# Kernel optimization log

Hardware: AMD Instinct MI355X
Metric: run time of the kernel (lower is better)

Reference implementation:

```python
import jax, jax.numpy as jnp
import numpy as np

B, H, S, D = 1, 16, 2048, 64

def setup_inputs() -> dict:
    key = jax.random.key(0)
    kq, kk, kv = jax.random.split(key, 3)
    q = jax.random.normal(kq, (B, H, S, D), dtype=jnp.float32)
    k = jax.random.normal(kk, (B, H, S, D), dtype=jnp.float32)
    v = jax.random.normal(kv, (B, H, S, D), dtype=jnp.float32)
    return {"q": q, "k": k, "v": v}

def reference(q, k, v):
    # Non-flash Attend forward: causal=True, no mask/bias/prev_attn, dropout=0 (eval)
    dtype = q.dtype
    scale = q.shape[-1] ** -0.5
    # dots: [b, h, i, j]
    dots = jnp.einsum('bhid,bhjd->bhij', q, k) * scale
    i = dots.shape[-2]
    j = dots.shape[-1]
    # create_casual_mask: triu(j - i + 1) -> True where j_idx > i_idx + (j - i)
    causal_mask = jnp.triu(jnp.ones((i, j), dtype=bool), k=j - i + 1)
    mask_value = -jnp.finfo(dtype).max
    dots = jnp.where(causal_mask, mask_value, dots)
    # attn_fn = softmax in float32 (qk_norm=False), cast back to input dtype
    attn = jax.nn.softmax(dots.astype(jnp.float32), axis=-1).astype(dtype)
    out = jnp.einsum('bhij,bhjd->bhid', attn, v)
    return out
```

## Files before the change

### kernel.cpp

```cpp
#include <hip/hip_runtime.h>
#include <hip/hip_bf16.h>
#include <math.h>

#define SEQ 2048
#define NH  16
#define HD  64
#define NW  4

typedef __attribute__((ext_vector_type(8)))  short bf16x8;
typedef __attribute__((ext_vector_type(4)))  float f32x4;
typedef __attribute__((ext_vector_type(16))) float f32x16;

static __device__ inline short f2bf(float f) {
  union { float f; unsigned u; } x; x.f = f;
  unsigned u = x.u;
  unsigned r = (u + 0x7fffu + ((u >> 16) & 1u)) >> 16;
  return (short)r;
}
static __device__ inline unsigned pack2(float e, float o) {
  union { __hip_bfloat162 h; unsigned u; } c;
  c.h = __float22bfloat162_rn(make_float2(e, o));
  return c.u;
}
static __device__ inline bf16x8 cvt8(float4 a, float4 b) {
  union { __hip_bfloat162 h[4]; bf16x8 v; } u;
  u.h[0] = __float22bfloat162_rn(make_float2(a.x, a.y));
  u.h[1] = __float22bfloat162_rn(make_float2(a.z, a.w));
  u.h[2] = __float22bfloat162_rn(make_float2(b.x, b.y));
  u.h[3] = __float22bfloat162_rn(make_float2(b.z, b.w));
  return u.v;
}

__global__ __launch_bounds__(256) void conv_kv_kernel(
    const float* __restrict__ K, const float* __restrict__ V,
    short* __restrict__ Kf, short* __restrict__ Vf) {
  __shared__ short tile[64][72];
  const int h = blockIdx.y;
  const int t64 = blockIdx.x;
  const int tid = threadIdx.x;
  const int c = tid >> 6;
  const int lane = tid & 63;
  const int ql = lane & 31;
  const int hi = lane >> 5;

#pragma unroll
  for (int half = 0; half < 2; ++half) {
    const int t32 = t64 * 2 + half;
    const float* src = K + ((size_t)(h * SEQ + t32 * 32 + ql)) * HD + c * 16 + hi * 8;
    float4 a = *(const float4*)src;
    float4 b = *(const float4*)(src + 4);
    *(bf16x8*)(Kf + (((size_t)(h * 64 + t32) * 4 + c) * 64 + lane) * 8) = cvt8(a, b);
  }
  {
    const int r = tid >> 2, c0 = (tid & 3) * 16;
    const float* vs = V + ((size_t)(h * SEQ + t64 * 64 + r)) * HD + c0;
    float4 a0 = *(const float4*)(vs);
    float4 b0 = *(const float4*)(vs + 4);
    float4 a1 = *(const float4*)(vs + 8);
    float4 b1 = *(const float4*)(vs + 12);
    *(bf16x8*)&tile[r][c0]     = cvt8(a0, b0);
    *(bf16x8*)&tile[r][c0 + 8] = cvt8(a1, b1);
  }
  __syncthreads();
#pragma unroll
  for (int dt = 0; dt < 2; ++dt) {
    const int d = dt * 32 + ql;
    bf16x8 o;
#pragma unroll
    for (int j = 0; j < 8; ++j) o[j] = tile[c * 16 + hi * 8 + j][d];
    *(bf16x8*)(Vf + ((((size_t)(h * 32 + t64) * 2 + dt) * 4 + c) * 64 + lane) * 8) = o;
  }
}

__global__ __launch_bounds__(256, 4) void attn_fwd_kernel(
    const float* __restrict__ Q, const short* __restrict__ Kf,
    const short* __restrict__ Vf, float* __restrict__ Out) {
  const int tid = threadIdx.x;
  const int w = tid >> 6;
  const int lane = tid & 63;
  const int ql = lane & 31;
  const int hi = lane >> 5;

  const int id = blockIdx.x;
  const int x = id & 7;
  const int j = id >> 3;
  const int h = 2 * x + (j & 1);
  const int b = j >> 1;
  const int cc = b & 15;
  const int t = b >> 4;
  const int g = cc + ((t >> 1) << 4);
  const int qt = (t & 1) ? 63 - g : g;

  const int q0 = qt * 32;
  const size_t hqb = (size_t)h * SEQ * HD;

  __shared__ float lds_part[NW * 32][65];
  __shared__ float lds_l[NW][2][32];

  const float QSCALE = 0.125f * 1.4426950408889634f;
  bf16x8 qa[4];
  {
    const float* qbase = Q + hqb + (size_t)(q0 + ql) * HD + 8 * hi;
#pragma unroll
    for (int c = 0; c < 4; ++c) {
      const float* p = qbase + 16 * c;
      float4 a4 = *(const float4*)p;
      float4 b4 = *(const float4*)(p + 4);
      bf16x8 tt;
      tt[0] = f2bf(a4.x * QSCALE); tt[1] = f2bf(a4.y * QSCALE);
      tt[2] = f2bf(a4.z * QSCALE); tt[3] = f2bf(a4.w * QSCALE);
      tt[4] = f2bf(b4.x * QSCALE); tt[5] = f2bf(b4.y * QSCALE);
      tt[6] = f2bf(b4.z * QSCALE); tt[7] = f2bf(b4.w * QSCALE);
      qa[c] = tt;
    }
  }

  f32x16 ot0, ot1;
#pragma unroll
  for (int r = 0; r < 16; ++r) { ot0[r] = 0.f; ot1[r] = 0.f; }
  float ll = 0.f;

  const int n32 = qt + 1;
  for (int t32 = w; t32 < n32; t32 += NW) {
    const short* kbase = Kf + ((size_t)(h * 64 + t32) * 4) * 512 + lane * 8;
    bf16x8 kb[4];
#pragma unroll
    for (int c = 0; c < 4; ++c) kb[c] = *(const bf16x8*)(kbase + c * 512);

    const int t64 = t32 >> 1, ccb = (t32 & 1) * 2;
    const short* vbase = Vf + (((size_t)(h * 32 + t64) * 2) * 4 + ccb) * 512 + lane * 8;
    bf16x8 va0[2], va1[2];
    va0[0] = *(const bf16x8*)(vbase);
    va0[1] = *(const bf16x8*)(vbase + 512);
    va1[0] = *(const bf16x8*)(vbase + 2048);
    va1[1] = *(const bf16x8*)(vbase + 2048 + 512);

    f32x16 st;
#pragma unroll
    for (int r = 0; r < 16; ++r) st[r] = 0.f;
#pragma unroll
    for (int c = 0; c < 4; ++c)
      st = __builtin_amdgcn_mfma_f32_32x32x16_bf16(kb[c], qa[c], st, 0, 0, 0);

    if (t32 == n32 - 1) {
      const int qg = q0 + ql;
#pragma unroll
      for (int r = 0; r < 16; ++r) {
        int kv = t32 * 32 + (r & 3) + 8 * (r >> 2) + 4 * hi;
        if (kv > qg) st[r] = -INFINITY;
      }
    }

    float rs = 0.f;
    unsigned pk[8];
#pragma unroll
    for (int mm = 0; mm < 8; ++mm) {
      float a0 = exp2f(st[2 * mm]);
      float a1 = exp2f(st[2 * mm + 1]);
      rs += a0 + a1;
      pk[mm] = pack2(a0, a1);
    }
    ll += rs;

    {
      union { unsigned u[4]; bf16x8 v; } pb;
      auto r0 = __builtin_amdgcn_permlane32_swap((int)pk[0], (int)pk[2], false, false);
      auto r1 = __builtin_amdgcn_permlane32_swap((int)pk[1], (int)pk[3], false, false);
      pb.u[0] = (unsigned)r0[0]; pb.u[2] = (unsigned)r0[1];
      pb.u[1] = (unsigned)r1[0]; pb.u[3] = (unsigned)r1[1];
      ot0 = __builtin_amdgcn_mfma_f32_32x32x16_bf16(va0[0], pb.v, ot0, 0, 0, 0);
      ot1 = __builtin_amdgcn_mfma_f32_32x32x16_bf16(va1[0], pb.v, ot1, 0, 0, 0);
      auto r2 = __builtin_amdgcn_permlane32_swap((int)pk[4], (int)pk[6], false, false);
      auto r3 = __builtin_amdgcn_permlane32_swap((int)pk[5], (int)pk[7], false, false);
      pb.u[0] = (unsigned)r2[0]; pb.u[2] = (unsigned)r2[1];
      pb.u[1] = (unsigned)r3[0]; pb.u[3] = (unsigned)r3[1];
      ot0 = __builtin_amdgcn_mfma_f32_32x32x16_bf16(va0[1], pb.v, ot0, 0, 0, 0);
      ot1 = __builtin_amdgcn_mfma_f32_32x32x16_bf16(va1[1], pb.v, ot1, 0, 0, 0);
    }
  }

#pragma unroll
  for (int r = 0; r < 16; ++r) {
    lds_part[w * 32 + r][lane] = ot0[r];
    lds_part[w * 32 + 16 + r][lane] = ot1[r];
  }
  lds_l[w][hi][ql] = ll;
  __syncthreads();

  {
    const int q = w * 8 + (lane >> 3);
    const int db = (lane & 7) * 8;
    float lt = 0.f;
#pragma unroll
    for (int wv = 0; wv < NW; ++wv)
      lt += lds_l[wv][0][q] + lds_l[wv][1][q];
    float inv = 1.f / lt;
    float od[8];
#pragma unroll
    for (int j2 = 0; j2 < 8; ++j2) {
      int d = db + j2;
      int tile = d >> 5, dd = d & 31;
      int hid = (dd >> 2) & 1;
      int r = (dd & 3) + 4 * (dd >> 3);
      int row0 = tile * 16 + r;
      int col = q + 32 * hid;
      float acc = 0.f;
#pragma unroll
      for (int wv = 0; wv < NW; ++wv)
        acc += lds_part[wv * 32 + row0][col];
      od[j2] = acc * inv;
    }
    float* outp = Out + hqb + (size_t)(q0 + q) * HD + db;
    *(f32x4*)(outp)     = (f32x4){od[0], od[1], od[2], od[3]};
    *(f32x4*)(outp + 4) = (f32x4){od[4], od[5], od[6], od[7]};
  }
}

__global__ __launch_bounds__(64) void attn_fwd_fallback(
    const float* __restrict__ Q, const float* __restrict__ K,
    const float* __restrict__ V, float* __restrict__ Out) {
  const int lane = threadIdx.x & 63;
  const int lr = lane & 15;
  const int lg = lane >> 4;
  const int q0 = blockIdx.x * 16;
  const size_t hb = (size_t)blockIdx.y * SEQ * HD;
  const float LOG2E = 1.4426950408889634f;

  bf16x8 qa[2];
  {
    const float* qrow = Q + hb + (size_t)(q0 + lr) * HD;
#pragma unroll
    for (int dh = 0; dh < 2; ++dh) {
      const float* p = qrow + dh * 32 + lg * 8;
      bf16x8 t;
#pragma unroll
      for (int i = 0; i < 8; ++i) t[i] = f2bf(p[i] * 0.125f);
      qa[dh] = t;
    }
  }
  f32x4 o[4];
#pragma unroll
  for (int dt = 0; dt < 4; ++dt) o[dt] = (f32x4){0.f, 0.f, 0.f, 0.f};
  float m[4], ll[4];
#pragma unroll
  for (int r = 0; r < 4; ++r) { m[r] = -INFINITY; ll[r] = 0.f; }
  __shared__ float plds[16][33];
  const int nsteps = (q0 + 16 + 31) >> 5;
  for (int s = 0; s < nsteps; ++s) {
    const int k0 = s * 32;
    bf16x8 kb[2][2];
#pragma unroll
    for (int ct = 0; ct < 2; ++ct) {
      const float* krow = K + hb + (size_t)(k0 + ct * 16 + lr) * HD;
#pragma unroll
      for (int dh = 0; dh < 2; ++dh) {
        const float* p = krow + dh * 32 + lg * 8;
        bf16x8 t;
#pragma unroll
        for (int i = 0; i < 8; ++i) t[i] = f2bf(p[i]);
        kb[ct][dh] = t;
      }
    }
    f32x4 sc[2];
#pragma unroll
    for (int ct = 0; ct < 2; ++ct) {
      f32x4 z = (f32x4){0.f, 0.f, 0.f, 0.f};
      z = __builtin_amdgcn_mfma_f32_16x16x32_bf16(qa[0], kb[ct][0], z, 0, 0, 0);
      z = __builtin_amdgcn_mfma_f32_16x16x32_bf16(qa[1], kb[ct][1], z, 0, 0, 0);
      sc[ct] = z;
    }
    if (s == nsteps - 1) {
#pragma unroll
      for (int ct = 0; ct < 2; ++ct)
#pragma unroll
        for (int r = 0; r < 4; ++r) {
          int col = k0 + ct * 16 + lr;
          int row = q0 + 4 * lg + r;
          if (col > row) sc[ct][r] = -INFINITY;
        }
    }
    float mx[4];
#pragma unroll
    for (int r = 0; r < 4; ++r) mx[r] = fmaxf(sc[0][r], sc[1][r]);
#pragma unroll
    for (int off = 1; off < 16; off <<= 1)
#pragma unroll
      for (int r = 0; r < 4; ++r) mx[r] = fmaxf(mx[r], __shfl_xor(mx[r], off, 64));
    float fac[4], pr[2][4], rs[4];
#pragma unroll
    for (int r = 0; r < 4; ++r) {
      float mn = fmaxf(m[r], mx[r]);
      fac[r] = exp2f((m[r] - mn) * LOG2E);
      m[r] = mn;
      float sum = 0.f;
#pragma unroll
      for (int ct = 0; ct < 2; ++ct) {
        float p = exp2f((sc[ct][r] - mn) * LOG2E);
        pr[ct][r] = p;
        sum += p;
      }
      rs[r] = sum;
    }
#pragma unroll
    for (int off = 1; off < 16; off <<= 1)
#pragma unroll
      for (int r = 0; r < 4; ++r) rs[r] += __shfl_xor(rs[r], off, 64);
#pragma unroll
    for (int r = 0; r < 4; ++r) ll[r] = ll[r] * fac[r] + rs[r];
#pragma unroll
    for (int dt = 0; dt < 4; ++dt)
#pragma unroll
      for (int r = 0; r < 4; ++r) o[dt][r] *= fac[r];
    __syncthreads();
#pragma unroll
    for (int ct = 0; ct < 2; ++ct)
#pragma unroll
      for (int r = 0; r < 4; ++r)
        plds[4 * lg + r][ct * 16 + lr] = pr[ct][r];
    __syncthreads();
    bf16x8 pa;
    {
      const float* p = &plds[lr][lg * 8];
#pragma unroll
      for (int i = 0; i < 8; ++i) pa[i] = f2bf(p[i]);
    }
#pragma unroll
    for (int dt = 0; dt < 4; ++dt) {
      const float* vcol = V + hb + (size_t)(k0 + lg * 8) * HD + dt * 16 + lr;
      bf16x8 vb;
#pragma unroll
      for (int i = 0; i < 8; ++i) vb[i] = f2bf(vcol[(size_t)i * HD]);
      o[dt] = __builtin_amdgcn_mfma_f32_16x16x32_bf16(pa, vb, o[dt], 0, 0, 0);
    }
  }
#pragma unroll
  for (int dt = 0; dt < 4; ++dt)
#pragma unroll
    for (int r = 0; r < 4; ++r) {
      int row = q0 + 4 * lg + r;
      Out[hb + (size_t)row * HD + dt * 16 + lr] = o[dt][r] / ll[r];
    }
}

extern "C" void kernel_launch(void* const* d_in, const int* in_sizes, int n_in,
                              void* d_out, int out_size, void* d_ws, size_t ws_size,
                              hipStream_t stream) {
  const float* q = (const float*)d_in[0];
  const float* k = (const float*)d_in[1];
  const float* v = (const float*)d_in[2];
  float* out = (float*)d_out;

  const size_t elems = (size_t)NH * SEQ * HD;
  const size_t need = 2 * elems * sizeof(short);

  if (ws_size >= need) {
    short* Kf = (short*)d_ws;
    short* Vf = Kf + elems;
    conv_kv_kernel<<<dim3(SEQ / 64, NH), 256, 0, stream>>>(k, v, Kf, Vf);
    attn_fwd_kernel<<<dim3((SEQ / 32) * NH), 256, 0, stream>>>(q, Kf, Vf, out);
  } else {
    attn_fwd_fallback<<<dim3(SEQ / 16, NH), dim3(64), 0, stream>>>(q, k, v, out);
  }
}
```

Baseline: 32.80 us.

## Prefetch next K/V tile into per-wave LDS staging with async global_load_lds

Each wave now issues asynchronous global-to-LDS loads for its next K/V tile, using a per-wave staging buffer that aliases the reduction scratch space. It then reads the current tile from LDS into registers before the MFMA work. The aim is to hide global load latency behind the QK and PV compute of the current tile, where before each iteration's loads were exposed. In exchange it adds LDS round-trips, explicit waitcnt barriers and a `__syncthreads` before the aliased reduction buffer is reused.

```diff
diff --git a/kernel.cpp b/kernel.cpp
--- a/kernel.cpp
+++ b/kernel.cpp
@@ -10,6 +10,9 @@
 typedef __attribute__((ext_vector_type(8)))  short bf16x8;
 typedef __attribute__((ext_vector_type(4)))  float f32x4;
 typedef __attribute__((ext_vector_type(16))) float f32x16;
+
+typedef unsigned __attribute__((address_space(1))) gu32;
+typedef unsigned __attribute__((address_space(3))) lu32;
 
 static __device__ inline short f2bf(float f) {
   union { float f; unsigned u; } x; x.f = f;
@@ -29,6 +32,9 @@
   u.h[2] = __float22bfloat162_rn(make_float2(b.x, b.y));
   u.h[3] = __float22bfloat162_rn(make_float2(b.z, b.w));
   return u.v;
+}
+static __device__ __forceinline__ void gload16(const short* g, short* l) {
+  __builtin_amdgcn_global_load_lds((const gu32*)g, (lu32*)l, 16, 0, 0);
 }
 
 __global__ __launch_bounds__(256) void conv_kv_kernel(
@@ -94,8 +100,10 @@
   const int q0 = qt * 32;
   const size_t hqb = (size_t)h * SEQ * HD;
 
-  __shared__ float lds_part[NW * 32][65];
-  __shared__ float lds_l[NW][2][32];
+  __shared__ __align__(16) char smem[34304];
+  float (*lds_part)[65] = (float(*)[65])smem;
+  float (*lds_l)[2][32] = (float(*)[2][32])(smem + 33280);
+  short* stageW = (short*)(smem + w * 8192);
 
   const float QSCALE = 0.125f * 1.4426950408889634f;
   bf16x8 qa[4];
@@ -121,19 +129,38 @@
   float ll = 0.f;
 
   const int n32 = qt + 1;
+
+  auto issue_tile = [&](int t32) {
+    const short* kg = Kf + ((size_t)(h * 64 + t32) * 4) * 512 + lane * 8;
+#pragma unroll
+    for (int c = 0; c < 4; ++c) gload16(kg + c * 512, stageW + c * 512);
+    const int t64 = t32 >> 1, ccb = (t32 & 1) * 2;
+    const short* vg = Vf + (((size_t)(h * 32 + t64) * 2) * 4 + ccb) * 512 + lane * 8;
+    gload16(vg,              stageW + 2048);
+    gload16(vg + 512,        stageW + 2048 + 512);
+    gload16(vg + 2048,       stageW + 2048 + 1024);
+    gload16(vg + 2048 + 512, stageW + 2048 + 1536);
+  };
+
+  if (w < n32) issue_tile(w);
+  asm volatile("s_waitcnt vmcnt(0)" ::: "memory");
+
   for (int t32 = w; t32 < n32; t32 += NW) {
-    const short* kbase = Kf + ((size_t)(h * 64 + t32) * 4) * 512 + lane * 8;
     bf16x8 kb[4];
 #pragma unroll
-    for (int c = 0; c < 4; ++c) kb[c] = *(const bf16x8*)(kbase + c * 512);
-
-    const int t64 = t32 >> 1, ccb = (t32 & 1) * 2;
-    const short* vbase = Vf + (((size_t)(h * 32 + t64) * 2) * 4 + ccb) * 512 + lane * 8;
+    for (int c = 0; c < 4; ++c)
+      kb[c] = *(const bf16x8*)(stageW + c * 512 + lane * 8);
     bf16x8 va0[2], va1[2];
-    va0[0] = *(const bf16x8*)(vbase);
-    va0[1] = *(const bf16x8*)(vbase + 512);
-    va1[0] = *(const bf16x8*)(vbase + 2048);
-    va1[1] = *(const bf16x8*)(vbase + 2048 + 512);
+    va0[0] = *(const bf16x8*)(stageW + 2048 + lane * 8);
+    va0[1] = *(const bf16x8*)(stageW + 2048 + 512 + lane * 8);
+    va1[0] = *(const bf16x8*)(stageW + 2048 + 1024 + lane * 8);
+    va1[1] = *(const bf16x8*)(stageW + 2048 + 1536 + lane * 8);
+
+    asm volatile("s_waitcnt lgkmcnt(0)" ::: "memory");
+    __builtin_amdgcn_sched_barrier(0);
+
+    const int tn = t32 + NW;
+    if (tn < n32) issue_tile(tn);
 
     f32x16 st;
 #pragma unroll
@@ -177,7 +204,11 @@
       ot0 = __builtin_amdgcn_mfma_f32_32x32x16_bf16(va0[1], pb.v, ot0, 0, 0, 0);
       ot1 = __builtin_amdgcn_mfma_f32_32x32x16_bf16(va1[1], pb.v, ot1, 0, 0, 0);
     }
-  }
+
+    asm volatile("s_waitcnt vmcnt(0)" ::: "memory");
+  }
+
+  __syncthreads();
 
 #pragma unroll
   for (int r = 0; r < 16; ++r) {
```

New measurement: 35.68 us. +8.8%, slower.
